# Kernel optimization log

Measured on AMD Instinct MI355X. Metric: run time of the kernel, lower is better.

## Reference

```python
import jax, jax.numpy as jnp
import numpy as np

HID = 64
HEADS = 4
HEAD_DIM = HID // HEADS
N_MOL, N_PROT = 2048, 4096
E_MOL, E_PROT = 32768, 131072
B = 32


def _lin(key, din, dout):
    kw, kb = jax.random.split(key)
    s = 1.0 / np.sqrt(din)
    W = jax.random.uniform(kw, (din, dout), jnp.float32, -s, s)
    b = jax.random.uniform(kb, (dout,), jnp.float32, -s, s)
    return W, b


def setup_inputs() -> dict:
    key = jax.random.key(0)
    ks = jax.random.split(key, 32)
    inp = {}
    inp['mol_x'] = jax.random.normal(ks[0], (N_MOL, 11), jnp.float32)
    inp['prot_x'] = jax.random.normal(ks[1], (N_PROT, 15), jnp.float32)
    inp['mol_eattr'] = jax.random.normal(ks[2], (E_MOL, 10), jnp.float32)
    inp['prot_eattr'] = jax.random.normal(ks[3], (E_PROT, 10), jnp.float32)
    inp['mol_edge_index'] = jax.random.randint(ks[4], (2, E_MOL), 0, N_MOL, jnp.int32)
    inp['prot_edge_index'] = jax.random.randint(ks[5], (2, E_PROT), 0, N_PROT, jnp.int32)
    inp['mol_batch'] = jnp.sort(jax.random.randint(ks[6], (N_MOL,), 0, B, jnp.int32))
    inp['prot_batch'] = jnp.sort(jax.random.randint(ks[7], (N_PROT,), 0, B, jnp.int32))
    inp['node_lin_mol_W'], inp['node_lin_mol_b'] = _lin(ks[8], 11, HID)
    inp['node_lin_prot_W'], inp['node_lin_prot_b'] = _lin(ks[9], 15, HID)
    inp['edge_lin_mol_W'], inp['edge_lin_mol_b'] = _lin(ks[10], 10, HID)
    inp['edge_lin_prot_W'], inp['edge_lin_prot_b'] = _lin(ks[11], 10, HID)
    for pref, base in (('mol_conv', 12), ('prot_conv', 15)):
        W1s, b1s, W2s, b2s = [], [], [], []
        for l in range(3):
            k1, k2 = jax.random.split(ks[base + l])
            W1, b1 = _lin(k1, HID, HID)
            W2, b2 = _lin(k2, HID, HID)
            W1s.append(W1); b1s.append(b1); W2s.append(W2); b2s.append(b2)
        inp[pref + '_W1'] = jnp.stack(W1s); inp[pref + '_b1'] = jnp.stack(b1s)
        inp[pref + '_W2'] = jnp.stack(W2s); inp[pref + '_b2'] = jnp.stack(b2s)
    for pref, base in (('attn_mp', 18), ('attn_pm', 21)):
        Ws, bs = [], []
        for i in range(3):  # Q, K, V
            W, b = _lin(ks[base + i], HID, HID)
            Ws.append(W); bs.append(b)
        inp[pref + '_W'] = jnp.stack(Ws); inp[pref + '_b'] = jnp.stack(bs)
    inp['fc1_W'], inp['fc1_b'] = _lin(ks[24], 2 * HID, HID)
    inp['fc2_W'], inp['fc2_b'] = _lin(ks[25], HID, 1)
    return inp


def _gine_layer(x, src, dst, eattr, W1, b1, W2, b2):
    # message: ReLU(x_j + e_ji); GINEConv sum aggregation; eps = 0
    msg = jax.nn.relu(x[src] + eattr)                       # [E, H]
    agg = jax.ops.segment_sum(msg, dst, num_segments=x.shape[0])
    h = x + agg
    h = jax.nn.relu(h @ W1 + b1) @ W2 + b2                  # inner MLP
    return jax.nn.relu(h)                                   # post-conv ReLU


def _cross_attn(qn, kn, W, b):
    Nq, Nk = qn.shape[0], kn.shape[0]
    Q = (qn @ W[0] + b[0]).reshape(Nq, HEADS, HEAD_DIM)
    K = (kn @ W[1] + b[1]).reshape(Nk, HEADS, HEAD_DIM)
    V = (kn @ W[2] + b[2]).reshape(Nk, HEADS, HEAD_DIM)
    scores = jnp.einsum('qhd,khd->hqk', Q, K) / np.sqrt(HEAD_DIM)
    w = jax.nn.softmax(scores, axis=-1)
    out = jnp.einsum('hqk,khd->qhd', w, V)
    return out.reshape(Nq, HID)


def _pool(H, batch):
    s = jax.ops.segment_sum(H, batch, num_segments=B)
    c = jax.ops.segment_sum(jnp.ones((H.shape[0],), H.dtype), batch, num_segments=B)
    return s / jnp.maximum(c, 1.0)[:, None]


def _forward(mol_x, prot_x, mol_eattr, prot_eattr,
             node_lin_mol_W, node_lin_mol_b, node_lin_prot_W, node_lin_prot_b,
             edge_lin_mol_W, edge_lin_mol_b, edge_lin_prot_W, edge_lin_prot_b,
             mol_conv_W1, mol_conv_b1, mol_conv_W2, mol_conv_b2,
             prot_conv_W1, prot_conv_b1, prot_conv_W2, prot_conv_b2,
             attn_mp_W, attn_mp_b, attn_pm_W, attn_pm_b,
             fc1_W, fc1_b, fc2_W, fc2_b,
             mol_edge_index, prot_edge_index, mol_batch, prot_batch):
    xm = mol_x @ node_lin_mol_W + node_lin_mol_b
    xp = prot_x @ node_lin_prot_W + node_lin_prot_b
    em = mol_eattr @ edge_lin_mol_W + edge_lin_mol_b
    ep = prot_eattr @ edge_lin_prot_W + edge_lin_prot_b
    ms, md = mol_edge_index[0], mol_edge_index[1]
    ps, pd = prot_edge_index[0], prot_edge_index[1]
    for l in range(3):
        xm = _gine_layer(xm, ms, md, em, mol_conv_W1[l], mol_conv_b1[l], mol_conv_W2[l], mol_conv_b2[l])
    for l in range(3):
        xp = _gine_layer(xp, ps, pd, ep, prot_conv_W1[l], prot_conv_b1[l], prot_conv_W2[l], prot_conv_b2[l])
    H_mol = xm + _cross_attn(xm, xp, attn_mp_W, attn_mp_b)
    H_prot = xp + _cross_attn(xp, xm, attn_pm_W, attn_pm_b)
    z = jnp.concatenate([_pool(H_mol, mol_batch), _pool(H_prot, prot_batch)], axis=1)
    h = jax.nn.relu(z @ fc1_W + fc1_b)
    return jax.nn.sigmoid(h @ fc2_W + fc2_b).squeeze(-1)


def reference(mol_x, prot_x, mol_eattr, prot_eattr,
              node_lin_mol_W, node_lin_mol_b, node_lin_prot_W, node_lin_prot_b,
              edge_lin_mol_W, edge_lin_mol_b, edge_lin_prot_W, edge_lin_prot_b,
              mol_conv_W1, mol_conv_b1, mol_conv_W2, mol_conv_b2,
              prot_conv_W1, prot_conv_b1, prot_conv_W2, prot_conv_b2,
              attn_mp_W, attn_mp_b, attn_pm_W, attn_pm_b,
              fc1_W, fc1_b, fc2_W, fc2_b,
              mol_edge_index, prot_edge_index, mol_batch, prot_batch):
    return _forward(mol_x, prot_x, mol_eattr, prot_eattr,
                    node_lin_mol_W, node_lin_mol_b, node_lin_prot_W, node_lin_prot_b,
                    edge_lin_mol_W, edge_lin_mol_b, edge_lin_prot_W, edge_lin_prot_b,
                    mol_conv_W1, mol_conv_b1, mol_conv_W2, mol_conv_b2,
                    prot_conv_W1, prot_conv_b1, prot_conv_W2, prot_conv_b2,
                    attn_mp_W, attn_mp_b, attn_pm_W, attn_pm_b,
                    fc1_W, fc1_b, fc2_W, fc2_b,
                    mol_edge_index, prot_edge_index, mol_batch, prot_batch)
```

## Files before the change

### kernel.cpp

```cpp
#include <hip/hip_runtime.h>
#include <math.h>

#define HID 64
#define HEADS 4
#define HDIM 16
#define N_MOL 2048
#define N_PROT 4096
#define E_MOL 32768
#define E_PROT 131072
#define BATCH 32
#define N_TOT (N_MOL + N_PROT)
#define E_TOT (E_MOL + E_PROT)
#define CAP 128

#define TQA 16
#define TKA 32
#define KSTA 68
#define CH_MOL 4
#define CH_PROT 2
#define KCHUNK 1024
#define NGRP_MOL (N_MOL / TQA)

#define DOT4(a, b) ((a).x*(b).x + (a).y*(b).y + (a).z*(b).z + (a).w*(b).w)
#define EXP2(x) __builtin_amdgcn_exp2f(x)

__global__ void k_nlb(const float* __restrict__ mol_x, const float* __restrict__ prot_x,
                      const float* __restrict__ Wm, const float* __restrict__ bm,
                      const float* __restrict__ Wp, const float* __restrict__ bp,
                      const int* __restrict__ mol_ei, const int* __restrict__ prot_ei,
                      float* __restrict__ xm, float* __restrict__ xp,
                      int* __restrict__ cursor, int* __restrict__ eidx) {
    if (blockIdx.x < N_TOT / 4) {
        int w = threadIdx.x >> 6, t = threadIdx.x & 63;
        int n = blockIdx.x * 4 + w;
        if (n < N_MOL) {
            const float* xr = mol_x + n * 11;
            float acc = bm[t];
#pragma unroll
            for (int i = 0; i < 11; ++i) acc += xr[i] * Wm[i * HID + t];
            xm[n * HID + t] = acc;
        } else {
            int p = n - N_MOL;
            const float* xr = prot_x + p * 15;
            float acc = bp[t];
#pragma unroll
            for (int i = 0; i < 15; ++i) acc += xr[i] * Wp[i * HID + t];
            xp[p * HID + t] = acc;
        }
    } else {
        int e = (blockIdx.x - N_TOT / 4) * 256 + threadIdx.x;
        int node, loc;
        if (e < E_MOL) { node = mol_ei[E_MOL + e]; loc = e; }
        else { int el = e - E_MOL; node = N_MOL + prot_ei[E_PROT + el]; loc = el; }
        int pos = atomicAdd(&cursor[node], 1);
        eidx[(size_t)node * CAP + pos] = loc;
    }
}

__global__ __launch_bounds__(256, 4) void k_gine(
    const float* __restrict__ xin_m, const float* __restrict__ xin_p,
    float* __restrict__ xout_m, float* __restrict__ xout_p,
    const float* __restrict__ mol_ea, const float* __restrict__ prot_ea,
    const int* __restrict__ mol_ei, const int* __restrict__ prot_ei,
    const float* __restrict__ Wem, const float* __restrict__ bem,
    const float* __restrict__ Wep, const float* __restrict__ bep,
    const float* __restrict__ W1m, const float* __restrict__ b1m,
    const float* __restrict__ W2m, const float* __restrict__ b2m,
    const float* __restrict__ W1p, const float* __restrict__ b1p,
    const float* __restrict__ W2p, const float* __restrict__ b2p,
    const int* __restrict__ cnt, const int* __restrict__ eidx,
    int doProj,
    const float* __restrict__ mpW, const float* __restrict__ mpb,
    const float* __restrict__ pmW, const float* __restrict__ pmb,
    float* __restrict__ Qm, float* __restrict__ Kp, float* __restrict__ Vp,
    float* __restrict__ Qp, float* __restrict__ Km, float* __restrict__ Vm) {
    __shared__ float h0[4][HID];
    __shared__ float h1[4][HID];
    int w = threadIdx.x >> 6, t = threadIdx.x & 63;
    int nb = blockIdx.x * 4 + w;
    bool isMol = nb < N_MOL;
    const float* x  = isMol ? xin_m : xin_p;
    float* xo       = isMol ? xout_m : xout_p;
    const float* We = isMol ? Wem : Wep;
    float bt        = isMol ? bem[t] : bep[t];
    const float* ea_base = isMol ? mol_ea : prot_ea;
    const int* srcarr    = isMol ? mol_ei : prot_ei;
    int n0 = isMol ? nb : nb - N_MOL;
    float wcol[10];
#pragma unroll
    for (int i = 0; i < 10; ++i) wcol[i] = We[i * HID + t];

    int deg = cnt[nb];
    const int* lst = eidx + (size_t)nb * CAP;
    float agg = 0.f;
    int j = 0;
    for (; j + 4 <= deg; j += 4) {
        int4 e4 = *(const int4*)(lst + j);
        int s0 = srcarr[e4.x], s1 = srcarr[e4.y];
        int s2 = srcarr[e4.z], s3 = srcarr[e4.w];
        const float2* p0 = (const float2*)(ea_base + (size_t)e4.x * 10);
        const float2* p1 = (const float2*)(ea_base + (size_t)e4.y * 10);
        const float2* p2 = (const float2*)(ea_base + (size_t)e4.z * 10);
        const float2* p3 = (const float2*)(ea_base + (size_t)e4.w * 10);
        float2 a0 = p0[0], a1 = p0[1], a2 = p0[2], a3 = p0[3], a4 = p0[4];
        float2 b0 = p1[0], b1 = p1[1], b2 = p1[2], b3 = p1[3], b4 = p1[4];
        float2 c0 = p2[0], c1 = p2[1], c2 = p2[2], c3 = p2[3], c4 = p2[4];
        float2 d0_ = p3[0], d1_ = p3[1], d2_ = p3[2], d3_ = p3[3], d4_ = p3[4];
        float xs0 = x[(size_t)s0 * HID + t];
        float xs1 = x[(size_t)s1 * HID + t];
        float xs2 = x[(size_t)s2 * HID + t];
        float xs3 = x[(size_t)s3 * HID + t];
        float m0 = bt, m1 = bt, m2 = bt, m3 = bt;
        m0 = fmaf(a0.x, wcol[0], m0); m0 = fmaf(a0.y, wcol[1], m0);
        m0 = fmaf(a1.x, wcol[2], m0); m0 = fmaf(a1.y, wcol[3], m0);
        m0 = fmaf(a2.x, wcol[4], m0); m0 = fmaf(a2.y, wcol[5], m0);
        m0 = fmaf(a3.x, wcol[6], m0); m0 = fmaf(a3.y, wcol[7], m0);
        m0 = fmaf(a4.x, wcol[8], m0); m0 = fmaf(a4.y, wcol[9], m0);
        m1 = fmaf(b0.x, wcol[0], m1); m1 = fmaf(b0.y, wcol[1], m1);
        m1 = fmaf(b1.x, wcol[2], m1); m1 = fmaf(b1.y, wcol[3], m1);
        m1 = fmaf(b2.x, wcol[4], m1); m1 = fmaf(b2.y, wcol[5], m1);
        m1 = fmaf(b3.x, wcol[6], m1); m1 = fmaf(b3.y, wcol[7], m1);
        m1 = fmaf(b4.x, wcol[8], m1); m1 = fmaf(b4.y, wcol[9], m1);
        m2 = fmaf(c0.x, wcol[0], m2); m2 = fmaf(c0.y, wcol[1], m2);
        m2 = fmaf(c1.x, wcol[2], m2); m2 = fmaf(c1.y, wcol[3], m2);
        m2 = fmaf(c2.x, wcol[4], m2); m2 = fmaf(c2.y, wcol[5], m2);
        m2 = fmaf(c3.x, wcol[6], m2); m2 = fmaf(c3.y, wcol[7], m2);
        m2 = fmaf(c4.x, wcol[8], m2); m2 = fmaf(c4.y, wcol[9], m2);
        m3 = fmaf(d0_.x, wcol[0], m3); m3 = fmaf(d0_.y, wcol[1], m3);
        m3 = fmaf(d1_.x, wcol[2], m3); m3 = fmaf(d1_.y, wcol[3], m3);
        m3 = fmaf(d2_.x, wcol[4], m3); m3 = fmaf(d2_.y, wcol[5], m3);
        m3 = fmaf(d3_.x, wcol[6], m3); m3 = fmaf(d3_.y, wcol[7], m3);
        m3 = fmaf(d4_.x, wcol[8], m3); m3 = fmaf(d4_.y, wcol[9], m3);
        agg += (fmaxf(m0 + xs0, 0.f) + fmaxf(m1 + xs1, 0.f))
             + (fmaxf(m2 + xs2, 0.f) + fmaxf(m3 + xs3, 0.f));
    }
    for (; j < deg; ++j) {
        int e0 = lst[j];
        int s0 = srcarr[e0];
        const float2* p0 = (const float2*)(ea_base + (size_t)e0 * 10);
        float2 a0 = p0[0], a1 = p0[1], a2 = p0[2], a3 = p0[3], a4 = p0[4];
        float xs0 = x[(size_t)s0 * HID + t];
        float m0 = bt;
        m0 = fmaf(a0.x, wcol[0], m0); m0 = fmaf(a0.y, wcol[1], m0);
        m0 = fmaf(a1.x, wcol[2], m0); m0 = fmaf(a1.y, wcol[3], m0);
        m0 = fmaf(a2.x, wcol[4], m0); m0 = fmaf(a2.y, wcol[5], m0);
        m0 = fmaf(a3.x, wcol[6], m0); m0 = fmaf(a3.y, wcol[7], m0);
        m0 = fmaf(a4.x, wcol[8], m0); m0 = fmaf(a4.y, wcol[9], m0);
        agg += fmaxf(m0 + xs0, 0.f);
    }
    h0[w][t] = x[(size_t)n0 * HID + t] + agg;

    const float* W1 = isMol ? W1m : W1p;
    const float* W2 = isMol ? W2m : W2p;
    float b1v = isMol ? b1m[t] : b1p[t];
    float b2v = isMol ? b2m[t] : b2p[t];
    float acc0 = b1v;
    const float4* hA = (const float4*)h0[w];
#pragma unroll
    for (int k = 0; k < 16; ++k) {
        float4 a = hA[k];
        acc0 = fmaf(a.x, W1[(4 * k + 0) * HID + t], acc0);
        acc0 = fmaf(a.y, W1[(4 * k + 1) * HID + t], acc0);
        acc0 = fmaf(a.z, W1[(4 * k + 2) * HID + t], acc0);
        acc0 = fmaf(a.w, W1[(4 * k + 3) * HID + t], acc0);
    }
    h1[w][t] = fmaxf(acc0, 0.f);
    float d0 = b2v;
    const float4* gA = (const float4*)h1[w];
#pragma unroll
    for (int k = 0; k < 16; ++k) {
        float4 a = gA[k];
        d0 = fmaf(a.x, W2[(4 * k + 0) * HID + t], d0);
        d0 = fmaf(a.y, W2[(4 * k + 1) * HID + t], d0);
        d0 = fmaf(a.z, W2[(4 * k + 2) * HID + t], d0);
        d0 = fmaf(a.w, W2[(4 * k + 3) * HID + t], d0);
    }
    float xv0 = fmaxf(d0, 0.f);
    xo[(size_t)n0 * HID + t] = xv0;

    if (doProj) {
        h0[w][t] = xv0;
        const float *WQ, *bQ, *WK, *bK, *WV, *bV;
        float *dQ, *dK, *dV;
        if (isMol) { WQ = mpW;        bQ = mpb;       WK = pmW + 4096; bK = pmb + 64;
                     WV = pmW + 8192; bV = pmb + 128; dQ = Qm; dK = Km; dV = Vm; }
        else       { WQ = pmW;        bQ = pmb;       WK = mpW + 4096; bK = mpb + 64;
                     WV = mpW + 8192; bV = mpb + 128; dQ = Qp; dK = Kp; dV = Vp; }
        float aQ0 = bQ[t];
        float aK0 = bK[t];
        float aV0 = bV[t];
        const float4* rA = (const float4*)h0[w];
#pragma unroll
        for (int k = 0; k < 16; ++k) {
            float4 a = rA[k];
#pragma unroll
            for (int jj = 0; jj < 4; ++jj) {
                float av = (jj == 0) ? a.x : (jj == 1) ? a.y : (jj == 2) ? a.z : a.w;
                aQ0 = fmaf(av, WQ[(4 * k + jj) * HID + t], aQ0);
                aK0 = fmaf(av, WK[(4 * k + jj) * HID + t], aK0);
                aV0 = fmaf(av, WV[(4 * k + jj) * HID + t], aV0);
            }
        }
        dQ[(size_t)n0 * HID + t] = aQ0;
        dK[(size_t)n0 * HID + t] = aK0;
        dV[(size_t)n0 * HID + t] = aV0;
    }
}

__device__ inline void upd4(float4& A, const float4 v0, const float4 v1,
                            float p0, float p1, float al) {
    A.x = fmaf(p1, v1.x, fmaf(p0, v0.x, A.x * al));
    A.y = fmaf(p1, v1.y, fmaf(p0, v0.y, A.y * al));
    A.z = fmaf(p1, v1.z, fmaf(p0, v0.z, A.z * al));
    A.w = fmaf(p1, v1.w, fmaf(p0, v0.w, A.w * al));
}
__device__ inline void merge4(float4& A, const float4 B, float c1, float c2) {
    A.x = A.x * c1 + B.x * c2;
    A.y = A.y * c1 + B.y * c2;
    A.z = A.z * c1 + B.z * c2;
    A.w = A.w * c1 + B.w * c2;
}
__device__ inline float4 shfl4(const float4 a, int off) {
    float4 r;
    r.x = __shfl_xor(a.x, off, 64); r.y = __shfl_xor(a.y, off, 64);
    r.z = __shfl_xor(a.z, off, 64); r.w = __shfl_xor(a.w, off, 64);
    return r;
}

__global__ __launch_bounds__(256) void k_attn(
    const float* __restrict__ Qm, const float* __restrict__ Kp, const float* __restrict__ Vp,
    const float* __restrict__ Qp, const float* __restrict__ Km, const float* __restrict__ Vm,
    float* __restrict__ part_m, float* __restrict__ part_p) {
    __shared__ float Kl[2][TKA * KSTA];
    __shared__ float Vl[2][TKA * KSTA];

    int t = threadIdx.x;
    const float *Q, *K, *V;
    float* part;
    int q0, chunk, CH;
    {
        int b = blockIdx.x;
        const int MOLB = NGRP_MOL * CH_MOL;
        if (b < MOLB) {
            chunk = b & 3; q0 = (b >> 2) * TQA; CH = CH_MOL;
            Q = Qm; K = Kp; V = Vp; part = part_m;
        } else {
            b -= MOLB;
            chunk = b & 1; q0 = (b >> 1) * TQA; CH = CH_PROT;
            Q = Qp; K = Km; V = Vm; part = part_p;
        }
    }
    int kbeg = chunk * KCHUNK;

    int sub = t & 15, h = (t >> 4) & 3, qg = t >> 6;
    int r0 = t >> 4;
    int c0 = (t & 15) << 2;

    const float sc = 0.25f * 1.44269504088896f;
    float4 q4[4][4];
#pragma unroll
    for (int qq = 0; qq < 4; ++qq) {
        const float4* Qr = (const float4*)(Q + (q0 + qg * 4 + qq) * HID + h * HDIM);
#pragma unroll
        for (int j = 0; j < 4; ++j) {
            float4 v = Qr[j];
            v.x *= sc; v.y *= sc; v.z *= sc; v.w *= sc;
            q4[qq][j] = v;
        }
    }

    float mreg[4], lreg[4];
    float4 A[4][4];
#pragma unroll
    for (int qq = 0; qq < 4; ++qq) {
        mreg[qq] = -INFINITY; lreg[qq] = 0.f;
#pragma unroll
        for (int j = 0; j < 4; ++j) A[qq][j] = (float4){0.f, 0.f, 0.f, 0.f};
    }

    {
        const float4* Kg = (const float4*)(K + kbeg * HID);
        const float4* Vg = (const float4*)(V + kbeg * HID);
        float4 ka = Kg[t], kb = Kg[t + 256];
        float4 va = Vg[t], vb = Vg[t + 256];
        *(float4*)&Kl[0][r0 * KSTA + c0] = ka;
        *(float4*)&Kl[0][(r0 + 16) * KSTA + c0] = kb;
        *(float4*)&Vl[0][r0 * KSTA + c0] = va;
        *(float4*)&Vl[0][(r0 + 16) * KSTA + c0] = vb;
    }
    __syncthreads();

    const int NT = KCHUNK / TKA;
    for (int tile = 0; tile < NT; ++tile) {
        int cur = tile & 1;
        float4 ka, kb, va, vb;
        bool more = (tile + 1) < NT;
        if (more) {
            const float4* Kg = (const float4*)(K + (kbeg + (tile + 1) * TKA) * HID);
            const float4* Vg = (const float4*)(V + (kbeg + (tile + 1) * TKA) * HID);
            ka = Kg[t]; kb = Kg[t + 256];
            va = Vg[t]; vb = Vg[t + 256];
        }

        const float4* Kr0 = (const float4*)&Kl[cur][sub * KSTA + h * HDIM];
        const float4* Kr1 = (const float4*)&Kl[cur][(sub + 16) * KSTA + h * HDIM];
        float4 x0 = Kr0[0], x1 = Kr0[1], x2 = Kr0[2], x3 = Kr0[3];
        float4 y0 = Kr1[0], y1 = Kr1[1], y2 = Kr1[2], y3 = Kr1[3];

        float s0[4], s1[4];
#pragma unroll
        for (int qq = 0; qq < 4; ++qq) {
            s0[qq] = DOT4(x0, q4[qq][0]) + DOT4(x1, q4[qq][1]) + DOT4(x2, q4[qq][2]) + DOT4(x3, q4[qq][3]);
            s1[qq] = DOT4(y0, q4[qq][0]) + DOT4(y1, q4[qq][1]) + DOT4(y2, q4[qq][2]) + DOT4(y3, q4[qq][3]);
        }

        const float4* Vr0 = (const float4*)&Vl[cur][sub * KSTA + h * HDIM];
        const float4* Vr1 = (const float4*)&Vl[cur][(sub + 16) * KSTA + h * HDIM];
        float4 v00 = Vr0[0], v01 = Vr0[1], v02 = Vr0[2], v03 = Vr0[3];
        float4 v10 = Vr1[0], v11 = Vr1[1], v12 = Vr1[2], v13 = Vr1[3];

#pragma unroll
        for (int qq = 0; qq < 4; ++qq) {
            float mn = fmaxf(mreg[qq], fmaxf(s0[qq], s1[qq]));
            float al = EXP2(mreg[qq] - mn);
            float p0 = EXP2(s0[qq] - mn);
            float p1 = EXP2(s1[qq] - mn);
            lreg[qq] = lreg[qq] * al + p0 + p1;
            upd4(A[qq][0], v00, v10, p0, p1, al);
            upd4(A[qq][1], v01, v11, p0, p1, al);
            upd4(A[qq][2], v02, v12, p0, p1, al);
            upd4(A[qq][3], v03, v13, p0, p1, al);
            mreg[qq] = mn;
        }

        if (more) {
            int nxt = cur ^ 1;
            *(float4*)&Kl[nxt][r0 * KSTA + c0] = ka;
            *(float4*)&Kl[nxt][(r0 + 16) * KSTA + c0] = kb;
            *(float4*)&Vl[nxt][r0 * KSTA + c0] = va;
            *(float4*)&Vl[nxt][(r0 + 16) * KSTA + c0] = vb;
        }
        __syncthreads();
    }

#pragma unroll
    for (int off = 1; off < 16; off <<= 1) {
#pragma unroll
        for (int qq = 0; qq < 4; ++qq) {
            float m2 = __shfl_xor(mreg[qq], off, 64);
            float l2 = __shfl_xor(lreg[qq], off, 64);
            float4 B0 = shfl4(A[qq][0], off), B1 = shfl4(A[qq][1], off);
            float4 B2 = shfl4(A[qq][2], off), B3 = shfl4(A[qq][3], off);
            float mn = fmaxf(mreg[qq], m2);
            float c1 = EXP2(mreg[qq] - mn), c2 = EXP2(m2 - mn);
            lreg[qq] = lreg[qq] * c1 + l2 * c2;
            merge4(A[qq][0], B0, c1, c2); merge4(A[qq][1], B1, c1, c2);
            merge4(A[qq][2], B2, c1, c2); merge4(A[qq][3], B3, c1, c2);
            mreg[qq] = mn;
        }
    }

    if (sub == 0) {
#pragma unroll
        for (int qq = 0; qq < 4; ++qq) {
            int qi = q0 + qg * 4 + qq;
            float* pp = part + (size_t)((qi * HEADS + h) * CH + chunk) * 20;
            pp[0] = mreg[qq]; pp[1] = lreg[qq];
            *(float4*)&pp[4] = A[qq][0]; *(float4*)&pp[8] = A[qq][1];
            *(float4*)&pp[12] = A[qq][2]; *(float4*)&pp[16] = A[qq][3];
        }
    }
}

__global__ void k_pool(const float* __restrict__ part_m, const float* __restrict__ part_p,
                       const float* __restrict__ xm, const float* __restrict__ xp,
                       const int* __restrict__ mb, const int* __restrict__ pb,
                       float* __restrict__ pool, float* __restrict__ cnt) {
    __shared__ float sm[64][65];
    int b = blockIdx.x >> 3, sl = blockIdx.x & 7;
    int t = threadIdx.x;
    int h = t & 3, s = t >> 2;
    int ms, me, ps, pe;
    {
        int lo = 0, hi = N_MOL;
        while (lo < hi) { int mid = (lo + hi) >> 1; if (mb[mid] < b) lo = mid + 1; else hi = mid; }
        ms = lo; lo = ms; hi = N_MOL;
        while (lo < hi) { int mid = (lo + hi) >> 1; if (mb[mid] < b + 1) lo = mid + 1; else hi = mid; }
        me = lo;
        lo = 0; hi = N_PROT;
        while (lo < hi) { int mid = (lo + hi) >> 1; if (pb[mid] < b) lo = mid + 1; else hi = mid; }
        ps = lo; lo = ps; hi = N_PROT;
        while (lo < hi) { int mid = (lo + hi) >> 1; if (pb[mid] < b + 1) lo = mid + 1; else hi = mid; }
        pe = lo;
    }
    if (sl == 0 && t == 0) { cnt[b * 2] = (float)(me - ms); cnt[b * 2 + 1] = (float)(pe - ps); }

    {
        float acc[16];
#pragma unroll
        for (int d = 0; d < 16; ++d) acc[d] = 0.f;
        for (int q = ms + sl + 8 * s; q < me; q += 8 * 64) {
            const float* p0 = part_m + (size_t)(q * HEADS + h) * CH_MOL * 20;
            float mmax = -INFINITY;
#pragma unroll
            for (int c = 0; c < CH_MOL; ++c) mmax = fmaxf(mmax, p0[c * 20]);
            float lsum = 0.f, wgt[CH_MOL];
#pragma unroll
            for (int c = 0; c < CH_MOL; ++c) {
                wgt[c] = EXP2(p0[c * 20] - mmax);
                lsum += p0[c * 20 + 1] * wgt[c];
            }
            float inv = 1.f / lsum;
            const float* Xr = xm + q * HID + h * HDIM;
#pragma unroll
            for (int d = 0; d < 16; ++d) {
                float o = Xr[d];
#pragma unroll
                for (int c = 0; c < CH_MOL; ++c)
                    o = fmaf(p0[c * 20 + 4 + d], wgt[c] * inv, o);
                acc[d] += o;
            }
        }
#pragma unroll
        for (int d = 0; d < 16; ++d) sm[s][h * 16 + d] = acc[d];
    }
    __syncthreads();
    if (t < 64) {
        float sum = 0.f;
        for (int ss = 0; ss < 64; ++ss) sum += sm[ss][t];
        unsafeAtomicAdd(&pool[b * 128 + t], sum);
    }
    __syncthreads();

    {
        float acc[16];
#pragma unroll
        for (int d = 0; d < 16; ++d) acc[d] = 0.f;
        for (int q = ps + sl + 8 * s; q < pe; q += 8 * 64) {
            const float* p0 = part_p + (size_t)(q * HEADS + h) * CH_PROT * 20;
            float m0 = p0[0], m1 = p0[20];
            float mmax = fmaxf(m0, m1);
            float w0 = EXP2(m0 - mmax), w1 = EXP2(m1 - mmax);
            float inv = 1.f / (p0[1] * w0 + p0[21] * w1);
            w0 *= inv; w1 *= inv;
            const float* Xr = xp + q * HID + h * HDIM;
#pragma unroll
            for (int d = 0; d < 16; ++d)
                acc[d] += Xr[d] + p0[4 + d] * w0 + p0[24 + d] * w1;
        }
#pragma unroll
        for (int d = 0; d < 16; ++d) sm[s][h * 16 + d] = acc[d];
    }
    __syncthreads();
    if (t < 64) {
        float sum = 0.f;
        for (int ss = 0; ss < 64; ++ss) sum += sm[ss][t];
        unsafeAtomicAdd(&pool[b * 128 + 64 + t], sum);
    }
}

__global__ void k_head(const float* __restrict__ pool, const float* __restrict__ cnt,
                       const float* __restrict__ fc1W, const float* __restrict__ fc1b,
                       const float* __restrict__ fc2W, const float* __restrict__ fc2b,
                       float* __restrict__ out) {
    __shared__ float z[128];
    int b = blockIdx.x, t = threadIdx.x;
    float cm = fmaxf(cnt[b * 2 + 0], 1.f), cp = fmaxf(cnt[b * 2 + 1], 1.f);
    z[t] = pool[b * 128 + t] / cm;
    z[64 + t] = pool[b * 128 + 64 + t] / cp;
    __syncthreads();
    float acc = fc1b[t];
    const float4* zv = (const float4*)z;
#pragma unroll
    for (int k = 0; k < 32; ++k) {
        float4 hv = zv[k];
        acc = fmaf(hv.x, fc1W[(4 * k + 0) * 64 + t], acc);
        acc = fmaf(hv.y, fc1W[(4 * k + 1) * 64 + t], acc);
        acc = fmaf(hv.z, fc1W[(4 * k + 2) * 64 + t], acc);
        acc = fmaf(hv.w, fc1W[(4 * k + 3) * 64 + t], acc);
    }
    float hv = fmaxf(acc, 0.f);
    float prod = hv * fc2W[t];
#pragma unroll
    for (int off = 32; off > 0; off >>= 1) prod += __shfl_xor(prod, off, 64);
    if (t == 0) out[b] = 1.f / (1.f + __expf(-(prod + fc2b[0])));
}

extern "C" void kernel_launch(void* const* d_in, const int* in_sizes, int n_in,
                              void* d_out, int out_size, void* d_ws, size_t ws_size,
                              hipStream_t stream) {
    const float* mol_x   = (const float*)d_in[0];
    const float* prot_x  = (const float*)d_in[1];
    const float* mol_ea  = (const float*)d_in[2];
    const float* prot_ea = (const float*)d_in[3];
    const int*   mol_ei  = (const int*)d_in[4];
    const int*   prot_ei = (const int*)d_in[5];
    const int*   mol_b   = (const int*)d_in[6];
    const int*   prot_b  = (const int*)d_in[7];
    const float* nlmW = (const float*)d_in[8];
    const float* nlmb = (const float*)d_in[9];
    const float* nlpW = (const float*)d_in[10];
    const float* nlpb = (const float*)d_in[11];
    const float* elmW = (const float*)d_in[12];
    const float* elmb = (const float*)d_in[13];
    const float* elpW = (const float*)d_in[14];
    const float* elpb = (const float*)d_in[15];
    const float* mcW1 = (const float*)d_in[16];
    const float* mcb1 = (const float*)d_in[17];
    const float* mcW2 = (const float*)d_in[18];
    const float* mcb2 = (const float*)d_in[19];
    const float* pcW1 = (const float*)d_in[20];
    const float* pcb1 = (const float*)d_in[21];
    const float* pcW2 = (const float*)d_in[22];
    const float* pcb2 = (const float*)d_in[23];
    const float* mpW  = (const float*)d_in[24];
    const float* mpb  = (const float*)d_in[25];
    const float* pmW  = (const float*)d_in[26];
    const float* pmb  = (const float*)d_in[27];
    const float* fc1W = (const float*)d_in[28];
    const float* fc1b = (const float*)d_in[29];
    const float* fc2W = (const float*)d_in[30];
    const float* fc2b = (const float*)d_in[31];

    float* ws    = (float*)d_ws;
    float* xa_m  = ws;
    float* xa_p  = xa_m + 131072;
    float* xb_m  = xa_p + 262144;
    float* xb_p  = xb_m + 131072;
    float* Qm    = xb_p + 262144;
    float* Kp    = Qm + 131072;
    float* Vp    = Kp + 262144;
    float* Qp    = Vp + 262144;
    float* Km    = Qp + 262144;
    float* Vm    = Km + 131072;
    float* partm = Vm + 131072;
    float* partp = partm + 655360;
    int* cursor  = (int*)(partp + 655360);
    float* pool  = (float*)(cursor + N_TOT);
    float* cnt   = pool + 4096;
    int* eidx    = (int*)partm;

    hipMemsetAsync(cursor, 0, (size_t)(N_TOT + 4096 + 64) * 4, stream);

    k_nlb<<<N_TOT / 4 + E_TOT / 256, 256, 0, stream>>>(
        mol_x, prot_x, nlmW, nlmb, nlpW, nlpb, mol_ei, prot_ei, xa_m, xa_p, cursor, eidx);

    k_gine<<<N_TOT / 4, 256, 0, stream>>>(xa_m, xa_p, xb_m, xb_p, mol_ea, prot_ea, mol_ei, prot_ei,
        elmW, elmb, elpW, elpb,
        mcW1, mcb1, mcW2, mcb2, pcW1, pcb1, pcW2, pcb2, cursor, eidx,
        0, mpW, mpb, pmW, pmb, Qm, Kp, Vp, Qp, Km, Vm);
    k_gine<<<N_TOT / 4, 256, 0, stream>>>(xb_m, xb_p, xa_m, xa_p, mol_ea, prot_ea, mol_ei, prot_ei,
        elmW, elmb, elpW, elpb,
        mcW1 + 4096, mcb1 + 64, mcW2 + 4096, mcb2 + 64,
        pcW1 + 4096, pcb1 + 64, pcW2 + 4096, pcb2 + 64, cursor, eidx,
        0, mpW, mpb, pmW, pmb, Qm, Kp, Vp, Qp, Km, Vm);
    k_gine<<<N_TOT / 4, 256, 0, stream>>>(xa_m, xa_p, xb_m, xb_p, mol_ea, prot_ea, mol_ei, prot_ei,
        elmW, elmb, elpW, elpb,
        mcW1 + 8192, mcb1 + 128, mcW2 + 8192, mcb2 + 128,
        pcW1 + 8192, pcb1 + 128, pcW2 + 8192, pcb2 + 128, cursor, eidx,
        1, mpW, mpb, pmW, pmb, Qm, Kp, Vp, Qp, Km, Vm);

    k_attn<<<NGRP_MOL * CH_MOL + (N_PROT / TQA) * CH_PROT, 256, 0, stream>>>(
        Qm, Kp, Vp, Qp, Km, Vm, partm, partp);

    k_pool<<<BATCH * 8, 256, 0, stream>>>(partm, partp, xb_m, xb_p, mol_b, prot_b, pool, cnt);
    k_head<<<BATCH, 64, 0, stream>>>(pool, cnt, fc1W, fc1b, fc2W, fc2b, (float*)d_out);
}
```

Before: 347.4 us.

## Fuse node/edge setup and three GINE layers into one persistent kernel

Replaces the node-linear/bucketing kernel and the three per-layer GINE launches with a single persistent kernel of 1024 blocks that strides over nodes and separates the stages with software grid barriers built on atomic counters. The goal is to remove three kernel launch gaps and tail drains between dependent stages. In exchange it depends on all 1024 blocks being co-resident, or the spin barrier deadlocks. It also reduces parallelism per stage, since each wave now processes 1-2 nodes per layer, and adds spin-wait overhead plus extra memset bytes for the barrier counters.

```diff
diff --git a/kernel.cpp b/kernel.cpp
--- a/kernel.cpp
+++ b/kernel.cpp
@@ -21,63 +21,49 @@
 #define KCHUNK 1024
 #define NGRP_MOL (N_MOL / TQA)
 
+#define FRONT_BLKS 1024
+#define FRONT_WAVES (FRONT_BLKS * 4)
+
 #define DOT4(a, b) ((a).x*(b).x + (a).y*(b).y + (a).z*(b).z + (a).w*(b).w)
 #define EXP2(x) __builtin_amdgcn_exp2f(x)
 
-__global__ void k_nlb(const float* __restrict__ mol_x, const float* __restrict__ prot_x,
-                      const float* __restrict__ Wm, const float* __restrict__ bm,
-                      const float* __restrict__ Wp, const float* __restrict__ bp,
-                      const int* __restrict__ mol_ei, const int* __restrict__ prot_ei,
-                      float* __restrict__ xm, float* __restrict__ xp,
-                      int* __restrict__ cursor, int* __restrict__ eidx) {
-    if (blockIdx.x < N_TOT / 4) {
-        int w = threadIdx.x >> 6, t = threadIdx.x & 63;
-        int n = blockIdx.x * 4 + w;
-        if (n < N_MOL) {
-            const float* xr = mol_x + n * 11;
-            float acc = bm[t];
-#pragma unroll
-            for (int i = 0; i < 11; ++i) acc += xr[i] * Wm[i * HID + t];
-            xm[n * HID + t] = acc;
-        } else {
-            int p = n - N_MOL;
-            const float* xr = prot_x + p * 15;
-            float acc = bp[t];
-#pragma unroll
-            for (int i = 0; i < 15; ++i) acc += xr[i] * Wp[i * HID + t];
-            xp[p * HID + t] = acc;
-        }
-    } else {
-        int e = (blockIdx.x - N_TOT / 4) * 256 + threadIdx.x;
-        int node, loc;
-        if (e < E_MOL) { node = mol_ei[E_MOL + e]; loc = e; }
-        else { int el = e - E_MOL; node = N_MOL + prot_ei[E_PROT + el]; loc = el; }
-        int pos = atomicAdd(&cursor[node], 1);
-        eidx[(size_t)node * CAP + pos] = loc;
-    }
-}
-
-__global__ __launch_bounds__(256, 4) void k_gine(
-    const float* __restrict__ xin_m, const float* __restrict__ xin_p,
-    float* __restrict__ xout_m, float* __restrict__ xout_p,
-    const float* __restrict__ mol_ea, const float* __restrict__ prot_ea,
-    const int* __restrict__ mol_ei, const int* __restrict__ prot_ei,
-    const float* __restrict__ Wem, const float* __restrict__ bem,
-    const float* __restrict__ Wep, const float* __restrict__ bep,
-    const float* __restrict__ W1m, const float* __restrict__ b1m,
-    const float* __restrict__ W2m, const float* __restrict__ b2m,
-    const float* __restrict__ W1p, const float* __restrict__ b1p,
-    const float* __restrict__ W2p, const float* __restrict__ b2p,
-    const int* __restrict__ cnt, const int* __restrict__ eidx,
+struct FrontParams {
+    const float *mol_x, *prot_x, *mol_ea, *prot_ea;
+    const int   *mol_ei, *prot_ei;
+    const float *nlmW, *nlmb, *nlpW, *nlpb;
+    const float *elmW, *elmb, *elpW, *elpb;
+    const float *mcW1, *mcb1, *mcW2, *mcb2;
+    const float *pcW1, *pcb1, *pcW2, *pcb2;
+    const float *mpW, *mpb, *pmW, *pmb;
+    float *xa_m, *xa_p, *xb_m, *xb_p;
+    float *Qm, *Kp, *Vp, *Qp, *Km, *Vm;
+    int *cursor, *eidx, *bar;
+};
+
+__device__ __forceinline__ void gbar(int* b) {
+    __syncthreads();
+    if (threadIdx.x == 0) {
+        __threadfence();
+        atomicAdd(b, 1);
+        while (atomicAdd(b, 0) < FRONT_BLKS) __builtin_amdgcn_s_sleep(1);
+        __threadfence();
+    }
+    __syncthreads();
+}
+
+__device__ __forceinline__ void gine_node(
+    int nb, float* h0, float* h1, int t,
+    const float* xin_m, const float* xin_p,
+    float* xout_m, float* xout_p,
+    const float* mol_ea, const float* prot_ea,
+    const int* mol_ei, const int* prot_ei,
+    const float* Wem, const float* bem, const float* Wep, const float* bep,
+    const float* W1m, const float* b1m, const float* W2m, const float* b2m,
+    const float* W1p, const float* b1p, const float* W2p, const float* b2p,
+    const int* cnt, const int* eidx,
     int doProj,
-    const float* __restrict__ mpW, const float* __restrict__ mpb,
-    const float* __restrict__ pmW, const float* __restrict__ pmb,
-    float* __restrict__ Qm, float* __restrict__ Kp, float* __restrict__ Vp,
-    float* __restrict__ Qp, float* __restrict__ Km, float* __restrict__ Vm) {
-    __shared__ float h0[4][HID];
-    __shared__ float h1[4][HID];
-    int w = threadIdx.x >> 6, t = threadIdx.x & 63;
-    int nb = blockIdx.x * 4 + w;
+    const float* mpW, const float* mpb, const float* pmW, const float* pmb,
+    float* Qm, float* Kp, float* Vp, float* Qp, float* Km, float* Vm) {
     bool isMol = nb < N_MOL;
     const float* x  = isMol ? xin_m : xin_p;
     float* xo       = isMol ? xout_m : xout_p;
@@ -148,14 +134,14 @@
         m0 = fmaf(a4.x, wcol[8], m0); m0 = fmaf(a4.y, wcol[9], m0);
         agg += fmaxf(m0 + xs0, 0.f);
     }
-    h0[w][t] = x[(size_t)n0 * HID + t] + agg;
+    h0[t] = x[(size_t)n0 * HID + t] + agg;
 
     const float* W1 = isMol ? W1m : W1p;
     const float* W2 = isMol ? W2m : W2p;
     float b1v = isMol ? b1m[t] : b1p[t];
     float b2v = isMol ? b2m[t] : b2p[t];
     float acc0 = b1v;
-    const float4* hA = (const float4*)h0[w];
+    const float4* hA = (const float4*)h0;
 #pragma unroll
     for (int k = 0; k < 16; ++k) {
         float4 a = hA[k];
@@ -164,9 +150,9 @@
         acc0 = fmaf(a.z, W1[(4 * k + 2) * HID + t], acc0);
         acc0 = fmaf(a.w, W1[(4 * k + 3) * HID + t], acc0);
     }
-    h1[w][t] = fmaxf(acc0, 0.f);
+    h1[t] = fmaxf(acc0, 0.f);
     float d0 = b2v;
-    const float4* gA = (const float4*)h1[w];
+    const float4* gA = (const float4*)h1;
 #pragma unroll
     for (int k = 0; k < 16; ++k) {
         float4 a = gA[k];
@@ -179,7 +165,7 @@
     xo[(size_t)n0 * HID + t] = xv0;
 
     if (doProj) {
-        h0[w][t] = xv0;
+        h0[t] = xv0;
         const float *WQ, *bQ, *WK, *bK, *WV, *bV;
         float *dQ, *dK, *dV;
         if (isMol) { WQ = mpW;        bQ = mpb;       WK = pmW + 4096; bK = pmb + 64;
@@ -189,7 +175,7 @@
         float aQ0 = bQ[t];
         float aK0 = bK[t];
         float aV0 = bV[t];
-        const float4* rA = (const float4*)h0[w];
+        const float4* rA = (const float4*)h0;
 #pragma unroll
         for (int k = 0; k < 16; ++k) {
             float4 a = rA[k];
@@ -205,6 +191,72 @@
         dK[(size_t)n0 * HID + t] = aK0;
         dV[(size_t)n0 * HID + t] = aV0;
     }
+}
+
+__global__ __launch_bounds__(256, 4) void k_front(FrontParams p) {
+    __shared__ float h0[4][HID];
+    __shared__ float h1[4][HID];
+    int tid = threadIdx.x;
+    int t = tid & 63, w = tid >> 6;
+    int bid = blockIdx.x;
+    int gw = bid * 4 + w;
+
+    for (int n = gw; n < N_TOT; n += FRONT_WAVES) {
+        if (n < N_MOL) {
+            const float* xr = p.mol_x + n * 11;
+            float acc = p.nlmb[t];
+#pragma unroll
+            for (int i = 0; i < 11; ++i) acc += xr[i] * p.nlmW[i * HID + t];
+            p.xa_m[(size_t)n * HID + t] = acc;
+        } else {
+            int q = n - N_MOL;
+            const float* xr = p.prot_x + q * 15;
+            float acc = p.nlpb[t];
+#pragma unroll
+            for (int i = 0; i < 15; ++i) acc += xr[i] * p.nlpW[i * HID + t];
+            p.xa_p[(size_t)q * HID + t] = acc;
+        }
+    }
+    {
+        int e = bid * 256 + tid;
+        if (e < E_TOT) {
+            int node, loc;
+            if (e < E_MOL) { node = p.mol_ei[E_MOL + e]; loc = e; }
+            else { int el = e - E_MOL; node = N_MOL + p.prot_ei[E_PROT + el]; loc = el; }
+            int pos = atomicAdd(&p.cursor[node], 1);
+            p.eidx[(size_t)node * CAP + pos] = loc;
+        }
+    }
+    gbar(p.bar + 0);
+
+    for (int nb = gw; nb < N_TOT; nb += FRONT_WAVES)
+        gine_node(nb, h0[w], h1[w], t, p.xa_m, p.xa_p, p.xb_m, p.xb_p,
+                  p.mol_ea, p.prot_ea, p.mol_ei, p.prot_ei,
+                  p.elmW, p.elmb, p.elpW, p.elpb,
+                  p.mcW1, p.mcb1, p.mcW2, p.mcb2,
+                  p.pcW1, p.pcb1, p.pcW2, p.pcb2,
+                  p.cursor, p.eidx, 0, p.mpW, p.mpb, p.pmW, p.pmb,
+                  p.Qm, p.Kp, p.Vp, p.Qp, p.Km, p.Vm);
+    gbar(p.bar + 1);
+
+    for (int nb = gw; nb < N_TOT; nb += FRONT_WAVES)
+        gine_node(nb, h0[w], h1[w], t, p.xb_m, p.xb_p, p.xa_m, p.xa_p,
+                  p.mol_ea, p.prot_ea, p.mol_ei, p.prot_ei,
+                  p.elmW, p.elmb, p.elpW, p.elpb,
+                  p.mcW1 + 4096, p.mcb1 + 64, p.mcW2 + 4096, p.mcb2 + 64,
+                  p.pcW1 + 4096, p.pcb1 + 64, p.pcW2 + 4096, p.pcb2 + 64,
+                  p.cursor, p.eidx, 0, p.mpW, p.mpb, p.pmW, p.pmb,
+                  p.Qm, p.Kp, p.Vp, p.Qp, p.Km, p.Vm);
+    gbar(p.bar + 2);
+
+    for (int nb = gw; nb < N_TOT; nb += FRONT_WAVES)
+        gine_node(nb, h0[w], h1[w], t, p.xa_m, p.xa_p, p.xb_m, p.xb_p,
+                  p.mol_ea, p.prot_ea, p.mol_ei, p.prot_ei,
+                  p.elmW, p.elmb, p.elpW, p.elpb,
+                  p.mcW1 + 8192, p.mcb1 + 128, p.mcW2 + 8192, p.mcb2 + 128,
+                  p.pcW1 + 8192, p.pcb1 + 128, p.pcW2 + 8192, p.pcb2 + 128,
+                  p.cursor, p.eidx, 1, p.mpW, p.mpb, p.pmW, p.pmb,
+                  p.Qm, p.Kp, p.Vp, p.Qp, p.Km, p.Vm);
 }
 
 __device__ inline void upd4(float4& A, const float4 v0, const float4 v1,
@@ -538,27 +590,24 @@
     int* cursor  = (int*)(partp + 655360);
     float* pool  = (float*)(cursor + N_TOT);
     float* cnt   = pool + 4096;
+    int* bar     = (int*)(cnt + 64);
     int* eidx    = (int*)partm;
 
-    hipMemsetAsync(cursor, 0, (size_t)(N_TOT + 4096 + 64) * 4, stream);
-
-    k_nlb<<<N_TOT / 4 + E_TOT / 256, 256, 0, stream>>>(
-        mol_x, prot_x, nlmW, nlmb, nlpW, nlpb, mol_ei, prot_ei, xa_m, xa_p, cursor, eidx);
-
-    k_gine<<<N_TOT / 4, 256, 0, stream>>>(xa_m, xa_p, xb_m, xb_p, mol_ea, prot_ea, mol_ei, prot_ei,
-        elmW, elmb, elpW, elpb,
-        mcW1, mcb1, mcW2, mcb2, pcW1, pcb1, pcW2, pcb2, cursor, eidx,
-        0, mpW, mpb, pmW, pmb, Qm, Kp, Vp, Qp, Km, Vm);
-    k_gine<<<N_TOT / 4, 256, 0, stream>>>(xb_m, xb_p, xa_m, xa_p, mol_ea, prot_ea, mol_ei, prot_ei,
-        elmW, elmb, elpW, elpb,
-        mcW1 + 4096, mcb1 + 64, mcW2 + 4096, mcb2 + 64,
-        pcW1 + 4096, pcb1 + 64, pcW2 + 4096, pcb2 + 64, cursor, eidx,
-        0, mpW, mpb, pmW, pmb, Qm, Kp, Vp, Qp, Km, Vm);
-    k_gine<<<N_TOT / 4, 256, 0, stream>>>(xa_m, xa_p, xb_m, xb_p, mol_ea, prot_ea, mol_ei, prot_ei,
-        elmW, elmb, elpW, elpb,
-        mcW1 + 8192, mcb1 + 128, mcW2 + 8192, mcb2 + 128,
-        pcW1 + 8192, pcb1 + 128, pcW2 + 8192, pcb2 + 128, cursor, eidx,
-        1, mpW, mpb, pmW, pmb, Qm, Kp, Vp, Qp, Km, Vm);
+    hipMemsetAsync(cursor, 0, (size_t)(N_TOT + 4096 + 64 + 8) * 4, stream);
+
+    FrontParams P;
+    P.mol_x = mol_x; P.prot_x = prot_x; P.mol_ea = mol_ea; P.prot_ea = prot_ea;
+    P.mol_ei = mol_ei; P.prot_ei = prot_ei;
+    P.nlmW = nlmW; P.nlmb = nlmb; P.nlpW = nlpW; P.nlpb = nlpb;
+    P.elmW = elmW; P.elmb = elmb; P.elpW = elpW; P.elpb = elpb;
+    P.mcW1 = mcW1; P.mcb1 = mcb1; P.mcW2 = mcW2; P.mcb2 = mcb2;
+    P.pcW1 = pcW1; P.pcb1 = pcb1; P.pcW2 = pcW2; P.pcb2 = pcb2;
+    P.mpW = mpW; P.mpb = mpb; P.pmW = pmW; P.pmb = pmb;
+    P.xa_m = xa_m; P.xa_p = xa_p; P.xb_m = xb_m; P.xb_p = xb_p;
+    P.Qm = Qm; P.Kp = Kp; P.Vp = Vp; P.Qp = Qp; P.Km = Km; P.Vm = Vm;
+    P.cursor = cursor; P.eidx = eidx; P.bar = bar;
+
+    k_front<<<FRONT_BLKS, 256, 0, stream>>>(P);
 
     k_attn<<<NGRP_MOL * CH_MOL + (N_PROT / TQA) * CH_PROT, 256, 0, stream>>>(
         Qm, Kp, Vp, Qp, Km, Vm, partm, partp);
```

Measured after the change: 842.6 us. 143% more time.

## Read attention K/V tiles directly from global memory instead of LDS double-buffering

Applied to the files above, without the earlier changes.

The cross-attention kernel no longer stages K and V tiles through double-buffered shared memory. Each thread now loads its own K/V rows straight from global memory, relying on L1/L2 caching since the K/V set is small and shared across blocks. This removes the LDS writes and the per-tile __syncthreads, and launch bounds now request 4 blocks per CU to raise occupancy. In exchange there is more global/L1 traffic, with each K/V element read by several waves, and there is no explicit prefetch to hide latency.

```diff
diff --git a/kernel.cpp b/kernel.cpp
--- a/kernel.cpp
+++ b/kernel.cpp
@@ -15,7 +15,6 @@
 
 #define TQA 16
 #define TKA 32
-#define KSTA 68
 #define CH_MOL 4
 #define CH_PROT 2
 #define KCHUNK 1024
@@ -227,13 +226,10 @@
     return r;
 }
 
-__global__ __launch_bounds__(256) void k_attn(
+__global__ __launch_bounds__(256, 4) void k_attn(
     const float* __restrict__ Qm, const float* __restrict__ Kp, const float* __restrict__ Vp,
     const float* __restrict__ Qp, const float* __restrict__ Km, const float* __restrict__ Vm,
     float* __restrict__ part_m, float* __restrict__ part_p) {
-    __shared__ float Kl[2][TKA * KSTA];
-    __shared__ float Vl[2][TKA * KSTA];
-
     int t = threadIdx.x;
     const float *Q, *K, *V;
     float* part;
@@ -253,8 +249,6 @@
     int kbeg = chunk * KCHUNK;
 
     int sub = t & 15, h = (t >> 4) & 3, qg = t >> 6;
-    int r0 = t >> 4;
-    int c0 = (t & 15) << 2;
 
     const float sc = 0.25f * 1.44269504088896f;
     float4 q4[4][4];
@@ -278,32 +272,14 @@
         for (int j = 0; j < 4; ++j) A[qq][j] = (float4){0.f, 0.f, 0.f, 0.f};
     }
 
-    {
-        const float4* Kg = (const float4*)(K + kbeg * HID);
-        const float4* Vg = (const float4*)(V + kbeg * HID);
-        float4 ka = Kg[t], kb = Kg[t + 256];
-        float4 va = Vg[t], vb = Vg[t + 256];
-        *(float4*)&Kl[0][r0 * KSTA + c0] = ka;
-        *(float4*)&Kl[0][(r0 + 16) * KSTA + c0] = kb;
-        *(float4*)&Vl[0][r0 * KSTA + c0] = va;
-        *(float4*)&Vl[0][(r0 + 16) * KSTA + c0] = vb;
-    }
-    __syncthreads();
+    const float* Kbase = K + (size_t)kbeg * HID + sub * HID + h * HDIM;
+    const float* Vbase = V + (size_t)kbeg * HID + sub * HID + h * HDIM;
+    const int STEP = TKA * HID;
 
     const int NT = KCHUNK / TKA;
     for (int tile = 0; tile < NT; ++tile) {
-        int cur = tile & 1;
-        float4 ka, kb, va, vb;
-        bool more = (tile + 1) < NT;
-        if (more) {
-            const float4* Kg = (const float4*)(K + (kbeg + (tile + 1) * TKA) * HID);
-            const float4* Vg = (const float4*)(V + (kbeg + (tile + 1) * TKA) * HID);
-            ka = Kg[t]; kb = Kg[t + 256];
-            va = Vg[t]; vb = Vg[t + 256];
-        }
-
-        const float4* Kr0 = (const float4*)&Kl[cur][sub * KSTA + h * HDIM];
-        const float4* Kr1 = (const float4*)&Kl[cur][(sub + 16) * KSTA + h * HDIM];
+        const float4* Kr0 = (const float4*)(Kbase + tile * STEP);
+        const float4* Kr1 = (const float4*)(Kbase + tile * STEP + 16 * HID);
         float4 x0 = Kr0[0], x1 = Kr0[1], x2 = Kr0[2], x3 = Kr0[3];
         float4 y0 = Kr1[0], y1 = Kr1[1], y2 = Kr1[2], y3 = Kr1[3];
 
@@ -314,8 +290,8 @@
             s1[qq] = DOT4(y0, q4[qq][0]) + DOT4(y1, q4[qq][1]) + DOT4(y2, q4[qq][2]) + DOT4(y3, q4[qq][3]);
         }
 
-        const float4* Vr0 = (const float4*)&Vl[cur][sub * KSTA + h * HDIM];
-        const float4* Vr1 = (const float4*)&Vl[cur][(sub + 16) * KSTA + h * HDIM];
+        const float4* Vr0 = (const float4*)(Vbase + tile * STEP);
+        const float4* Vr1 = (const float4*)(Vbase + tile * STEP + 16 * HID);
         float4 v00 = Vr0[0], v01 = Vr0[1], v02 = Vr0[2], v03 = Vr0[3];
         float4 v10 = Vr1[0], v11 = Vr1[1], v12 = Vr1[2], v13 = Vr1[3];
 
@@ -332,15 +308,6 @@
             upd4(A[qq][3], v03, v13, p0, p1, al);
             mreg[qq] = mn;
         }
-
-        if (more) {
-            int nxt = cur ^ 1;
-            *(float4*)&Kl[nxt][r0 * KSTA + c0] = ka;
-            *(float4*)&Kl[nxt][(r0 + 16) * KSTA + c0] = kb;
-            *(float4*)&Vl[nxt][r0 * KSTA + c0] = va;
-            *(float4*)&Vl[nxt][(r0 + 16) * KSTA + c0] = vb;
-        }
-        __syncthreads();
     }
 
 #pragma unroll
```

After: 1.041 ms. 2.99x slower.
